# Performance work log

Measured on AMD Instinct MI355X. Metric: run time of the kernel, lower is better.

## Reference

```python
import jax, jax.numpy as jnp
import numpy as np

PROCESSING_STEPS = 3


def setup_inputs() -> dict:
    key = jax.random.key(0)
    ks = jax.random.split(key, 8)
    B, N, d = 1024, 128, 128
    y = jax.random.normal(ks[0], (B, N, d), dtype=jnp.float32)
    lengths = jax.random.randint(ks[1], (B,), 1, N + 1, dtype=jnp.int32)
    s = 0.05
    W_ih = jax.random.normal(ks[2], (4 * d, 2 * d), dtype=jnp.float32) * s
    W_hh = jax.random.normal(ks[3], (4 * d, d), dtype=jnp.float32) * s
    b_ih = jax.random.normal(ks[4], (4 * d,), dtype=jnp.float32) * s
    b_hh = jax.random.normal(ks[5], (4 * d,), dtype=jnp.float32) * s
    W_m = jax.random.normal(ks[6], (1, 2 * d), dtype=jnp.float32) * s
    b_m = jax.random.normal(ks[7], (1,), dtype=jnp.float32) * s
    mean = jnp.zeros((1,), jnp.float32)
    stddev = jnp.ones((1,), jnp.float32)
    return {"y": y, "lengths": lengths, "W_ih": W_ih, "W_hh": W_hh,
            "b_ih": b_ih, "b_hh": b_hh, "W_m": W_m, "b_m": b_m,
            "mean": mean, "stddev": stddev}


def reference(y, lengths, W_ih, W_hh, b_ih, b_hh, W_m, b_m, mean, stddev):
    # y: [B, N, d] padded atomwise representation; lengths: valid atoms per molecule
    B, N, d = y.shape
    mask = jnp.arange(N)[None, :] < lengths[:, None]          # [B, N]
    maskf = mask.astype(y.dtype)[..., None]                    # [B, N, 1]
    neg_inf = jnp.finfo(y.dtype).min

    q_star = jnp.zeros((B, 2 * d), y.dtype)
    h = jnp.zeros((B, d), y.dtype)
    c = jnp.zeros((B, d), y.dtype)

    def step(carry, _):
        q_star, h, c = carry
        # single-layer LSTM cell (PyTorch gate order i, f, g, o)
        gates = q_star @ W_ih.T + b_ih + h @ W_hh.T + b_hh     # [B, 4d]
        i, f, g, o = jnp.split(gates, 4, axis=-1)
        c2 = jax.nn.sigmoid(f) * c + jax.nn.sigmoid(i) * jnp.tanh(g)
        h2 = jax.nn.sigmoid(o) * jnp.tanh(c2)
        q = h2                                                  # [B, d]
        # attention: gather q per atom, segment softmax, scatter_add
        e = jnp.einsum('bnd,bd->bn', y, q)                      # [B, N]
        e = jnp.where(mask, e, neg_inf)
        a = jax.nn.softmax(e, axis=-1)[..., None] * maskf       # [B, N, 1]
        r = jnp.sum(a * y, axis=1)                              # [B, d]
        return (jnp.concatenate([q, r], axis=-1), h2, c2), None

    (q_star, h, c), _ = jax.lax.scan(step, (q_star, h, c), None,
                                     length=PROCESSING_STEPS)
    out = q_star @ W_m.T + b_m                                  # [B, 1]
    return out * stddev + mean
```

## Files before the change

### kernel.cpp

```cpp
#include <hip/hip_runtime.h>
#include <math.h>

#define BB 1024
#define NN 128
#define DD 128
#define GG 512

__device__ __forceinline__ float sigmoidf_(float x) { return 1.0f / (1.0f + expf(-x)); }

__global__ __launch_bounds__(256) void k_prep(
    const float* __restrict__ W_ih, const float* __restrict__ W_hh,
    const float* __restrict__ b_ih, const float* __restrict__ b_hh,
    float* __restrict__ Wc, float* __restrict__ biasv, float* __restrict__ gbase,
    float* __restrict__ h1, float* __restrict__ c1) {
  int b = blockIdx.x, t = threadIdx.x;
  if (b < 64) {
    int base = b * 1024;
    for (int i = t; i < 1024; i += 256) {
      int idx = base + i;
      int j = idx >> 7, d = idx & 127;
      Wc[idx] = W_ih[(j << 8) + d] + W_hh[idx];
    }
  } else {
    __shared__ float bv[GG];
    __shared__ float h1l[DD];
    for (int j = t; j < GG; j += 256) bv[j] = b_ih[j] + b_hh[j];
    __syncthreads();
    if (t < DD) {
      float cc = sigmoidf_(bv[t]) * tanhf(bv[256 + t]);
      float hh = sigmoidf_(bv[384 + t]) * tanhf(cc);
      h1l[t] = hh;
      if (b == 64) { c1[t] = cc; h1[t] = hh; }
    }
    if (b == 64) for (int j = t; j < GG; j += 256) biasv[j] = bv[j];
    __syncthreads();
    int j0 = (b - 64) * 128;
    if (t < 128) {
      int j = j0 + t;
      float acc = bv[j];
      const float* wi = W_ih + (j << 8);
      const float* wh = W_hh + (j << 7);
      #pragma unroll 8
      for (int d = 0; d < DD; ++d) acc = fmaf(wi[d] + wh[d], h1l[d], acc);
      gbase[j] = acc;
    }
  }
}

__global__ __launch_bounds__(256) void k_attn(
    const float* __restrict__ y, const int* __restrict__ lengths,
    const float* __restrict__ qsrc, int q_bcast,
    float* __restrict__ rT,
    const float* __restrict__ Wm, const float* __restrict__ bm,
    const float* __restrict__ mn, const float* __restrict__ sd,
    float* __restrict__ out, int is_final) {
  __shared__ float ql[DD];
  __shared__ float rp[16][DD];
  __shared__ float redm[4], reds[4], redf[4];

  int t = threadIdx.x, lane = t & 63, w = t >> 6;
  int sub = lane & 15, g = lane >> 4;
  int m = blockIdx.x;
  int len = lengths[m];
  const float* yb = y + (size_t)m * (NN * DD);
  int d0 = sub << 3;

  if (t < DD) ql[t] = q_bcast ? qsrc[t] : qsrc[t * BB + m];
  __syncthreads();

  float4 q0 = *(const float4*)&ql[d0];
  float4 q1 = *(const float4*)&ql[d0 + 4];

  float4 va[8], vb[8];
  float ee[8];
  int base_n = (w << 2) + g;

  #pragma unroll
  for (int it = 0; it < 8; ++it) {
    int n = (it << 4) + base_n;
    int nc = (n < len) ? n : (len - 1);
    const float4* yr = (const float4*)(yb + nc * DD + d0);
    va[it] = yr[0];
    vb[it] = yr[1];
    float p = fmaf(va[it].x, q0.x, fmaf(va[it].y, q0.y,
              fmaf(va[it].z, q0.z, fmaf(va[it].w, q0.w,
              fmaf(vb[it].x, q1.x, fmaf(vb[it].y, q1.y,
              fmaf(vb[it].z, q1.z, vb[it].w * q1.w)))))));
    #pragma unroll
    for (int s = 1; s < 16; s <<= 1) p += __shfl_xor(p, s, 64);
    ee[it] = (n < len) ? p : -3.0e38f;
  }

  float mloc = ee[0];
  #pragma unroll
  for (int it = 1; it < 8; ++it) mloc = fmaxf(mloc, ee[it]);
  #pragma unroll
  for (int s = 1; s < 64; s <<= 1) mloc = fmaxf(mloc, __shfl_xor(mloc, s, 64));
  if (lane == 0) redm[w] = mloc;
  __syncthreads();
  float mx = fmaxf(fmaxf(redm[0], redm[1]), fmaxf(redm[2], redm[3]));

  float a[8];
  float sl = 0.0f;
  #pragma unroll
  for (int it = 0; it < 8; ++it) { a[it] = expf(ee[it] - mx); sl += a[it]; }
  #pragma unroll
  for (int s = 1; s < 64; s <<= 1) sl += __shfl_xor(sl, s, 64);
  if (lane == 0) reds[w] = sl;
  __syncthreads();
  float invZ = 16.0f / (reds[0] + reds[1] + reds[2] + reds[3]);

  float4 r0 = {0.f, 0.f, 0.f, 0.f}, r1 = {0.f, 0.f, 0.f, 0.f};
  #pragma unroll
  for (int it = 0; it < 8; ++it) {
    float av = a[it];
    r0.x = fmaf(av, va[it].x, r0.x); r0.y = fmaf(av, va[it].y, r0.y);
    r0.z = fmaf(av, va[it].z, r0.z); r0.w = fmaf(av, va[it].w, r0.w);
    r1.x = fmaf(av, vb[it].x, r1.x); r1.y = fmaf(av, vb[it].y, r1.y);
    r1.z = fmaf(av, vb[it].z, r1.z); r1.w = fmaf(av, vb[it].w, r1.w);
  }
  int wg = (w << 2) | g;
  *(float4*)&rp[wg][d0] = r0;
  *(float4*)&rp[wg][d0 + 4] = r1;
  __syncthreads();

  float r_ = 0.0f;
  if (t < DD) {
    #pragma unroll
    for (int k = 0; k < 16; ++k) r_ += rp[k][t];
    r_ *= invZ;
    if (!is_final) rT[t * BB + m] = r_;
  }
  if (is_final) {
    float part = (t < DD) ? (Wm[t] * ql[t] + Wm[DD + t] * r_) : 0.0f;
    #pragma unroll
    for (int s = 1; s < 64; s <<= 1) part += __shfl_xor(part, s, 64);
    if (lane == 0) redf[w] = part;
    __syncthreads();
    if (t == 0) out[m] = (redf[0] + redf[1] + redf[2] + redf[3] + bm[0]) * sd[0] + mn[0];
  }
}

__global__ __launch_bounds__(512) void k_lstm(
    const float* __restrict__ W_ih, const float* __restrict__ Wc,
    const float* __restrict__ gb,
    const float* __restrict__ h_inT,
    const float* __restrict__ c_in, int c_bcast,
    const float* __restrict__ rT,
    float* __restrict__ h_outT, float* __restrict__ c_outT) {
  __shared__ float xl[DD * 64];
  int t = threadIdx.x;
  int ml = t & 63, wid = t >> 6;
  int m0 = blockIdx.x << 6;
  int m = m0 + ml;
  int jb = __builtin_amdgcn_readfirstlane((blockIdx.y << 3) + wid);

  float ai = gb[jb], af = gb[DD + jb], ag = gb[2 * DD + jb], ao = gb[3 * DD + jb];

  if (h_inT) {
    #pragma unroll
    for (int k = 0; k < 16; ++k) {
      int i = (k << 9) + t;
      xl[i] = h_inT[(i >> 6) * BB + m0 + (i & 63)];
    }
    __syncthreads();
    const float* w0 = Wc + jb * DD;
    const float* w1 = Wc + (128 + jb) * DD;
    const float* w2 = Wc + (256 + jb) * DD;
    const float* w3 = Wc + (384 + jb) * DD;
    #pragma unroll 8
    for (int d = 0; d < DD; ++d) {
      float xd = xl[(d << 6) + ml];
      ai = fmaf(w0[d], xd, ai); af = fmaf(w1[d], xd, af);
      ag = fmaf(w2[d], xd, ag); ao = fmaf(w3[d], xd, ao);
    }
    __syncthreads();
  }

  #pragma unroll
  for (int k = 0; k < 16; ++k) {
    int i = (k << 9) + t;
    xl[i] = rT[(i >> 6) * BB + m0 + (i & 63)];
  }
  __syncthreads();
  {
    const float* w0 = W_ih + jb * 256 + 128;
    const float* w1 = W_ih + (128 + jb) * 256 + 128;
    const float* w2 = W_ih + (256 + jb) * 256 + 128;
    const float* w3 = W_ih + (384 + jb) * 256 + 128;
    #pragma unroll 8
    for (int d = 0; d < DD; ++d) {
      float xd = xl[(d << 6) + ml];
      ai = fmaf(w0[d], xd, ai); af = fmaf(w1[d], xd, af);
      ag = fmaf(w2[d], xd, ag); ao = fmaf(w3[d], xd, ao);
    }
  }

  float cin = c_bcast ? c_in[jb] : c_in[jb * BB + m];
  float cc = fmaf(sigmoidf_(af), cin, sigmoidf_(ai) * tanhf(ag));
  float hh = sigmoidf_(ao) * tanhf(cc);
  h_outT[jb * BB + m] = hh;
  if (c_outT) c_outT[jb * BB + m] = cc;
}

extern "C" void kernel_launch(void* const* d_in, const int* in_sizes, int n_in,
                              void* d_out, int out_size, void* d_ws, size_t ws_size,
                              hipStream_t stream) {
  const float* y    = (const float*)d_in[0];
  const int*   len  = (const int*)  d_in[1];
  const float* W_ih = (const float*)d_in[2];
  const float* W_hh = (const float*)d_in[3];
  const float* b_ih = (const float*)d_in[4];
  const float* b_hh = (const float*)d_in[5];
  const float* W_m  = (const float*)d_in[6];
  const float* b_m  = (const float*)d_in[7];
  const float* mean = (const float*)d_in[8];
  const float* sd   = (const float*)d_in[9];
  float* out = (float*)d_out;

  float* ws = (float*)d_ws;
  float* Wc    = ws;
  float* biasv = ws + 65536;
  float* gbase = ws + 66048;
  float* h1    = ws + 66560;
  float* c1    = ws + 66688;
  float* rT    = ws + 66816;
  float* h2T   = ws + 197888;
  float* c2T   = ws + 328960;
  float* h3T   = ws + 460032;

  k_prep<<<68, 256, 0, stream>>>(W_ih, W_hh, b_ih, b_hh, Wc, biasv, gbase, h1, c1);

  k_attn<<<BB, 256, 0, stream>>>(y, len, h1, 1, rT, W_m, b_m, mean, sd, nullptr, 0);
  k_lstm<<<dim3(16, 16), 512, 0, stream>>>(W_ih, Wc, gbase, nullptr, c1, 1, rT, h2T, c2T);
  k_attn<<<BB, 256, 0, stream>>>(y, len, h2T, 0, rT, W_m, b_m, mean, sd, nullptr, 0);
  k_lstm<<<dim3(16, 16), 512, 0, stream>>>(W_ih, Wc, biasv, h2T, c2T, 0, rT, h3T, nullptr);
  k_attn<<<BB, 256, 0, stream>>>(y, len, h3T, 0, nullptr, W_m, b_m, mean, sd, out, 1);
}
```

Measured before the change: 67.39 us.

## Skip padded rows in attention, single-barrier online softmax, row-major r/h layout

The attention kernel now skips loading and computing over groups of 4 rows that lie entirely past the molecule length. It replaces the two-barrier max/sum softmax with per-wave local max and sum merged through one barrier and rescaling. The partial r accumulation is reduced with shuffles before shared memory, so only 4 rows are stored instead of 16. The r and h buffers switch to a row-major [B,d] layout so the attention kernel reads and writes contiguously; the LSTM kernel transposes through padded shared memory to match. Risks include extra exp calls and the added transpose cost in the LSTM kernel.

```diff
diff --git a/kernel.cpp b/kernel.cpp
--- a/kernel.cpp
+++ b/kernel.cpp
@@ -50,12 +50,12 @@
 __global__ __launch_bounds__(256) void k_attn(
     const float* __restrict__ y, const int* __restrict__ lengths,
     const float* __restrict__ qsrc, int q_bcast,
-    float* __restrict__ rT,
+    float* __restrict__ rN,
     const float* __restrict__ Wm, const float* __restrict__ bm,
     const float* __restrict__ mn, const float* __restrict__ sd,
     float* __restrict__ out, int is_final) {
   __shared__ float ql[DD];
-  __shared__ float rp[16][DD];
+  __shared__ float rp[4][DD];
   __shared__ float redm[4], reds[4], redf[4];
 
   int t = threadIdx.x, lane = t & 63, w = t >> 6;
@@ -65,7 +65,7 @@
   const float* yb = y + (size_t)m * (NN * DD);
   int d0 = sub << 3;
 
-  if (t < DD) ql[t] = q_bcast ? qsrc[t] : qsrc[t * BB + m];
+  if (t < DD) ql[t] = q_bcast ? qsrc[t] : qsrc[m * DD + t];
   __syncthreads();
 
   float4 q0 = *(const float4*)&ql[d0];
@@ -73,22 +73,27 @@
 
   float4 va[8], vb[8];
   float ee[8];
-  int base_n = (w << 2) + g;
+  int wbase = w << 2;
 
   #pragma unroll
   for (int it = 0; it < 8; ++it) {
-    int n = (it << 4) + base_n;
-    int nc = (n < len) ? n : (len - 1);
-    const float4* yr = (const float4*)(yb + nc * DD + d0);
-    va[it] = yr[0];
-    vb[it] = yr[1];
-    float p = fmaf(va[it].x, q0.x, fmaf(va[it].y, q0.y,
-              fmaf(va[it].z, q0.z, fmaf(va[it].w, q0.w,
-              fmaf(vb[it].x, q1.x, fmaf(vb[it].y, q1.y,
-              fmaf(vb[it].z, q1.z, vb[it].w * q1.w)))))));
-    #pragma unroll
-    for (int s = 1; s < 16; s <<= 1) p += __shfl_xor(p, s, 64);
-    ee[it] = (n < len) ? p : -3.0e38f;
+    int nw = (it << 4) + wbase;
+    if (nw < len) {
+      int n = nw + g;
+      int nc = (n < len) ? n : (len - 1);
+      const float4* yr = (const float4*)(yb + nc * DD + d0);
+      va[it] = yr[0];
+      vb[it] = yr[1];
+      float p = fmaf(va[it].x, q0.x, fmaf(va[it].y, q0.y,
+                fmaf(va[it].z, q0.z, fmaf(va[it].w, q0.w,
+                fmaf(vb[it].x, q1.x, fmaf(vb[it].y, q1.y,
+                fmaf(vb[it].z, q1.z, vb[it].w * q1.w)))))));
+      #pragma unroll
+      for (int s = 1; s < 16; s <<= 1) p += __shfl_xor(p, s, 64);
+      ee[it] = (n < len) ? p : -3.0e38f;
+    } else {
+      ee[it] = -3.0e38f;
+    }
   }
 
   float mloc = ee[0];
@@ -96,40 +101,54 @@
   for (int it = 1; it < 8; ++it) mloc = fmaxf(mloc, ee[it]);
   #pragma unroll
   for (int s = 1; s < 64; s <<= 1) mloc = fmaxf(mloc, __shfl_xor(mloc, s, 64));
-  if (lane == 0) redm[w] = mloc;
-  __syncthreads();
-  float mx = fmaxf(fmaxf(redm[0], redm[1]), fmaxf(redm[2], redm[3]));
 
   float a[8];
   float sl = 0.0f;
   #pragma unroll
-  for (int it = 0; it < 8; ++it) { a[it] = expf(ee[it] - mx); sl += a[it]; }
+  for (int it = 0; it < 8; ++it) { a[it] = expf(ee[it] - mloc); sl += a[it]; }
   #pragma unroll
   for (int s = 1; s < 64; s <<= 1) sl += __shfl_xor(sl, s, 64);
-  if (lane == 0) reds[w] = sl;
-  __syncthreads();
-  float invZ = 16.0f / (reds[0] + reds[1] + reds[2] + reds[3]);
+  if (lane == 0) { redm[w] = mloc; reds[w] = sl; }
+  __syncthreads();
+
+  float m0_ = redm[0], m1_ = redm[1], m2_ = redm[2], m3_ = redm[3];
+  float mx = fmaxf(fmaxf(m0_, m1_), fmaxf(m2_, m3_));
+  float Zraw = reds[0] * expf(m0_ - mx) + reds[1] * expf(m1_ - mx) +
+               reds[2] * expf(m2_ - mx) + reds[3] * expf(m3_ - mx);
+  float wscale = expf(mloc - mx) * (16.0f / Zraw);
 
   float4 r0 = {0.f, 0.f, 0.f, 0.f}, r1 = {0.f, 0.f, 0.f, 0.f};
   #pragma unroll
   for (int it = 0; it < 8; ++it) {
-    float av = a[it];
-    r0.x = fmaf(av, va[it].x, r0.x); r0.y = fmaf(av, va[it].y, r0.y);
-    r0.z = fmaf(av, va[it].z, r0.z); r0.w = fmaf(av, va[it].w, r0.w);
-    r1.x = fmaf(av, vb[it].x, r1.x); r1.y = fmaf(av, vb[it].y, r1.y);
-    r1.z = fmaf(av, vb[it].z, r1.z); r1.w = fmaf(av, vb[it].w, r1.w);
-  }
-  int wg = (w << 2) | g;
-  *(float4*)&rp[wg][d0] = r0;
-  *(float4*)&rp[wg][d0 + 4] = r1;
+    int nw = (it << 4) + wbase;
+    if (nw < len) {
+      float av = a[it];
+      r0.x = fmaf(av, va[it].x, r0.x); r0.y = fmaf(av, va[it].y, r0.y);
+      r0.z = fmaf(av, va[it].z, r0.z); r0.w = fmaf(av, va[it].w, r0.w);
+      r1.x = fmaf(av, vb[it].x, r1.x); r1.y = fmaf(av, vb[it].y, r1.y);
+      r1.z = fmaf(av, vb[it].z, r1.z); r1.w = fmaf(av, vb[it].w, r1.w);
+    }
+  }
+  r0.x *= wscale; r0.y *= wscale; r0.z *= wscale; r0.w *= wscale;
+  r1.x *= wscale; r1.y *= wscale; r1.z *= wscale; r1.w *= wscale;
+
+  #pragma unroll
+  for (int s = 16; s < 64; s <<= 1) {
+    r0.x += __shfl_xor(r0.x, s, 64); r0.y += __shfl_xor(r0.y, s, 64);
+    r0.z += __shfl_xor(r0.z, s, 64); r0.w += __shfl_xor(r0.w, s, 64);
+    r1.x += __shfl_xor(r1.x, s, 64); r1.y += __shfl_xor(r1.y, s, 64);
+    r1.z += __shfl_xor(r1.z, s, 64); r1.w += __shfl_xor(r1.w, s, 64);
+  }
+  if (g == 0) {
+    *(float4*)&rp[w][d0] = r0;
+    *(float4*)&rp[w][d0 + 4] = r1;
+  }
   __syncthreads();
 
   float r_ = 0.0f;
   if (t < DD) {
-    #pragma unroll
-    for (int k = 0; k < 16; ++k) r_ += rp[k][t];
-    r_ *= invZ;
-    if (!is_final) rT[t * BB + m] = r_;
+    r_ = rp[0][t] + rp[1][t] + rp[2][t] + rp[3][t];
+    if (!is_final) rN[m * DD + t] = r_;
   }
   if (is_final) {
     float part = (t < DD) ? (Wm[t] * ql[t] + Wm[DD + t] * r_) : 0.0f;
@@ -144,11 +163,12 @@
 __global__ __launch_bounds__(512) void k_lstm(
     const float* __restrict__ W_ih, const float* __restrict__ Wc,
     const float* __restrict__ gb,
-    const float* __restrict__ h_inT,
+    const float* __restrict__ h_inN,
     const float* __restrict__ c_in, int c_bcast,
-    const float* __restrict__ rT,
-    float* __restrict__ h_outT, float* __restrict__ c_outT) {
-  __shared__ float xl[DD * 64];
+    const float* __restrict__ rNin,
+    float* __restrict__ h_outN, float* __restrict__ c_outT) {
+  __shared__ float xl[64 * 129];
+  __shared__ float ht[64 * 9];
   int t = threadIdx.x;
   int ml = t & 63, wid = t >> 6;
   int m0 = blockIdx.x << 6;
@@ -157,11 +177,12 @@
 
   float ai = gb[jb], af = gb[DD + jb], ag = gb[2 * DD + jb], ao = gb[3 * DD + jb];
 
-  if (h_inT) {
+  if (h_inN) {
     #pragma unroll
     for (int k = 0; k < 16; ++k) {
       int i = (k << 9) + t;
-      xl[i] = h_inT[(i >> 6) * BB + m0 + (i & 63)];
+      int mm = i >> 7, dd = i & 127;
+      xl[mm * 129 + dd] = h_inN[(m0 + mm) * DD + dd];
     }
     __syncthreads();
     const float* w0 = Wc + jb * DD;
@@ -170,7 +191,7 @@
     const float* w3 = Wc + (384 + jb) * DD;
     #pragma unroll 8
     for (int d = 0; d < DD; ++d) {
-      float xd = xl[(d << 6) + ml];
+      float xd = xl[ml * 129 + d];
       ai = fmaf(w0[d], xd, ai); af = fmaf(w1[d], xd, af);
       ag = fmaf(w2[d], xd, ag); ao = fmaf(w3[d], xd, ao);
     }
@@ -180,7 +201,8 @@
   #pragma unroll
   for (int k = 0; k < 16; ++k) {
     int i = (k << 9) + t;
-    xl[i] = rT[(i >> 6) * BB + m0 + (i & 63)];
+    int mm = i >> 7, dd = i & 127;
+    xl[mm * 129 + dd] = rNin[(m0 + mm) * DD + dd];
   }
   __syncthreads();
   {
@@ -190,7 +212,7 @@
     const float* w3 = W_ih + (384 + jb) * 256 + 128;
     #pragma unroll 8
     for (int d = 0; d < DD; ++d) {
-      float xd = xl[(d << 6) + ml];
+      float xd = xl[ml * 129 + d];
       ai = fmaf(w0[d], xd, ai); af = fmaf(w1[d], xd, af);
       ag = fmaf(w2[d], xd, ag); ao = fmaf(w3[d], xd, ao);
     }
@@ -199,8 +221,13 @@
   float cin = c_bcast ? c_in[jb] : c_in[jb * BB + m];
   float cc = fmaf(sigmoidf_(af), cin, sigmoidf_(ai) * tanhf(ag));
   float hh = sigmoidf_(ao) * tanhf(cc);
-  h_outT[jb * BB + m] = hh;
+  ht[ml * 9 + wid] = hh;
   if (c_outT) c_outT[jb * BB + m] = cc;
+  __syncthreads();
+  {
+    int jj = t & 7, mm = t >> 3;
+    h_outN[(m0 + mm) * DD + (blockIdx.y << 3) + jj] = ht[mm * 9 + jj];
+  }
 }
 
 extern "C" void kernel_launch(void* const* d_in, const int* in_sizes, int n_in,
@@ -224,16 +251,16 @@
   float* gbase = ws + 66048;
   float* h1    = ws + 66560;
   float* c1    = ws + 66688;
-  float* rT    = ws + 66816;
-  float* h2T   = ws + 197888;
+  float* rN    = ws + 66816;
+  float* h2N   = ws + 197888;
   float* c2T   = ws + 328960;
-  float* h3T   = ws + 460032;
+  float* h3N   = ws + 460032;
 
   k_prep<<<68, 256, 0, stream>>>(W_ih, W_hh, b_ih, b_hh, Wc, biasv, gbase, h1, c1);
 
-  k_attn<<<BB, 256, 0, stream>>>(y, len, h1, 1, rT, W_m, b_m, mean, sd, nullptr, 0);
-  k_lstm<<<dim3(16, 16), 512, 0, stream>>>(W_ih, Wc, gbase, nullptr, c1, 1, rT, h2T, c2T);
-  k_attn<<<BB, 256, 0, stream>>>(y, len, h2T, 0, rT, W_m, b_m, mean, sd, nullptr, 0);
-  k_lstm<<<dim3(16, 16), 512, 0, stream>>>(W_ih, Wc, biasv, h2T, c2T, 0, rT, h3T, nullptr);
-  k_attn<<<BB, 256, 0, stream>>>(y, len, h3T, 0, nullptr, W_m, b_m, mean, sd, out, 1);
-}
+  k_attn<<<BB, 256, 0, stream>>>(y, len, h1, 1, rN, W_m, b_m, mean, sd, nullptr, 0);
+  k_lstm<<<dim3(16, 16), 512, 0, stream>>>(W_ih, Wc, gbase, nullptr, c1, 1, rN, h2N, c2T);
+  k_attn<<<BB, 256, 0, stream>>>(y, len, h2N, 0, rN, W_m, b_m, mean, sd, nullptr, 0);
+  k_lstm<<<dim3(16, 16), 512, 0, stream>>>(W_ih, Wc, biasv, h2N, c2T, 0, rN, h3N, nullptr);
+  k_attn<<<BB, 256, 0, stream>>>(y, len, h3N, 0, nullptr, W_m, b_m, mean, sd, out, 1);
+}
```

After: 63.62 us. 5.6% less time.
